# Performance work log

Measured on AMD Instinct MI355X. Metric: run time of the kernel, lower is better.

Reference implementation:

```python
import jax, jax.numpy as jnp
import numpy as np

B, S, D, H = 4, 4096, 128, 128

def setup_inputs() -> dict:
    key = jax.random.key(0)
    ks = jax.random.split(key, 7)
    sd = 1.0 / np.sqrt(D)
    return {
        "x": jax.random.normal(ks[0], (B, S, D), dtype=jnp.float32),
        "Wq": jax.random.normal(ks[1], (D, H), dtype=jnp.float32) * sd,
        "bq": jax.random.normal(ks[2], (H,), dtype=jnp.float32) * sd,
        "Wk": jax.random.normal(ks[3], (D, H), dtype=jnp.float32) * sd,
        "bk": jax.random.normal(ks[4], (H,), dtype=jnp.float32) * sd,
        "Wv": jax.random.normal(ks[5], (D, D), dtype=jnp.float32) * sd,
        "bv": jax.random.normal(ks[6], (D,), dtype=jnp.float32) * sd,
    }

def reference(x, Wq, bq, Wk, bk, Wv, bv):
    # Q,K: [B,S,H]; V: [B,S,D]
    Q = jnp.einsum('bsd,dh->bsh', x, Wq) + bq
    K = jnp.einsum('bsd,dh->bsh', x, Wk) + bk
    V = jnp.einsum('bsd,de->bse', x, Wv) + bv
    scale = jnp.sqrt(jnp.asarray(H, dtype=x.dtype))
    scores = jnp.einsum('bqh,bkh->bqk', Q, K) / scale  # [B,S,S]
    attn = jax.nn.softmax(scores, axis=-1)             # dropout = identity (eval mode)
    context = jnp.einsum('bqk,bkd->bqd', attn, V)      # [B,S,D]
    return context.mean(axis=1)                        # [B,D]
```

## Files before the change

### kernel.cpp

```cpp
#include <hip/hip_runtime.h>

#define SLEN 4096
#define DDIM 128
#define BATCH 4
#define KROWS 256
#define NKB (SLEN / KROWS)
#define QROWS 256
#define NQR (SLEN / QROWS)
#define NW 8
#define SCLOG2E 0.12751743f

typedef __bf16 v8bf __attribute__((ext_vector_type(8)));
typedef float f32x4 __attribute__((ext_vector_type(4)));

__device__ __forceinline__ f32x4 mfma16(v8bf a, v8bf b, f32x4 c) {
  return __builtin_amdgcn_mfma_f32_16x16x32_bf16(a, b, c, 0, 0, 0);
}

__device__ __forceinline__ void gload_lds16(const void* g, void* l) {
  __builtin_amdgcn_global_load_lds(
      (const __attribute__((address_space(1))) unsigned int*)g,
      (__attribute__((address_space(3))) unsigned int*)l, 16, 0, 0);
}

__device__ __forceinline__ void decode_bid(int bid, int& b, int& qr, int& kblk) {
  int x = bid & 7;
  int i = bid >> 3;
  int pr = x * 8 + (i >> 4);
  kblk = i & 15;
  b = pr >> 4;
  qr = pr & 15;
}

__device__ __forceinline__ void stage_kslab(const __bf16* __restrict__ Krow0,
                                            char* buf, int wave, int lane) {
#pragma unroll
  for (int it = 0; it < 8; ++it) {
    int s = it * 512 + wave * 64 + lane;
    int r = s >> 4;
    int pp = s & 15;
    int lsl = pp ^ (r & 7);
    const __bf16* src = Krow0 + (size_t)r * DDIM + lsl * 8;
    char* dst = buf + (size_t)(it * 512 + wave * 64) * 16;
    gload_lds16(src, dst);
  }
}

__device__ __forceinline__ void read4(v8bf k[4], const char* const pa[4], int t) {
  int off = t << 12;
#pragma unroll
  for (int h = 0; h < 4; ++h)
    k[h] = *reinterpret_cast<const v8bf*>(pa[h] + off);
}

__device__ __forceinline__ void mfma8(f32x4 A[2], const v8bf qf[2][4],
                                      const v8bf k[4]) {
  A[0] = (f32x4){0.f, 0.f, 0.f, 0.f};
  A[1] = (f32x4){0.f, 0.f, 0.f, 0.f};
#pragma unroll
  for (int h = 0; h < 4; ++h) {
    A[0] = mfma16(qf[0][h], k[h], A[0]);
    A[1] = mfma16(qf[1][h], k[h], A[1]);
  }
}

__device__ __forceinline__ void consume_z(const f32x4 A[2], float zacc[2][4]) {
#pragma unroll
  for (int qs = 0; qs < 2; ++qs)
#pragma unroll
    for (int j = 0; j < 4; ++j)
      zacc[qs][j] += exp2f(A[qs][j]);
}

__global__ __launch_bounds__(256) void k1_proj(const float* __restrict__ x,
                                               const float* __restrict__ Wq,
                                               const float* __restrict__ Wk,
                                               const float* __restrict__ bq,
                                               const float* __restrict__ bk,
                                               __bf16* __restrict__ Qb,
                                               __bf16* __restrict__ Kb) {
  int wave = threadIdx.x >> 6, lane = threadIdx.x & 63;
  int lr = lane & 15, lg = lane >> 4;

  __shared__ __align__(16) char wlds[64 * 1024];

#pragma unroll
  for (int it = 0; it < 16; ++it) {
    int idx = it * 256 + threadIdx.x;
    int ct = idx >> 8;
    int hs = (idx >> 6) & 3;
    int l  = idx & 63;
    int col = ((ct & 7) << 4) + (l & 15);
    const float* W = (ct < 8) ? Wq : Wk;
    int hbase = hs * 32 + (l >> 4) * 8;
    v8bf t;
#pragma unroll
    for (int i = 0; i < 8; ++i)
      t[i] = (__bf16)W[(hbase + i) * DDIM + col];
    *reinterpret_cast<v8bf*>(wlds + (size_t)idx * 16) = t;
  }

  int r0 = blockIdx.x * 64 + wave * 16;
  const float* xrow = x + (size_t)(r0 + lr) * DDIM;

  v8bf xf[4];
#pragma unroll
  for (int hs = 0; hs < 4; ++hs) {
    float4 a = *reinterpret_cast<const float4*>(xrow + hs * 32 + lg * 8);
    float4 c = *reinterpret_cast<const float4*>(xrow + hs * 32 + lg * 8 + 4);
    v8bf t;
    t[0] = (__bf16)a.x; t[1] = (__bf16)a.y; t[2] = (__bf16)a.z; t[3] = (__bf16)a.w;
    t[4] = (__bf16)c.x; t[5] = (__bf16)c.y; t[6] = (__bf16)c.z; t[7] = (__bf16)c.w;
    xf[hs] = t;
  }

  __syncthreads();

  for (int ct = 0; ct < 16; ++ct) {
    f32x4 acc = {0.f, 0.f, 0.f, 0.f};
#pragma unroll
    for (int hs = 0; hs < 4; ++hs) {
      v8bf wf = *reinterpret_cast<const v8bf*>(
          wlds + (size_t)((ct * 4 + hs) * 64 + lane) * 16);
      acc = mfma16(xf[hs], wf, acc);
    }
    int col = ((ct & 7) << 4) + lr;
    float bias = (ct < 8) ? bq[col] : bk[col];
    float sc   = (ct < 8) ? SCLOG2E : 1.0f;
    __bf16* dst = (ct < 8) ? Qb : Kb;
#pragma unroll
    for (int j = 0; j < 4; ++j) {
      int row = r0 + lg * 4 + j;
      dst[(size_t)row * DDIM + col] = (__bf16)((acc[j] + bias) * sc);
    }
  }
}

__global__ __launch_bounds__(512, 4) void k2a_z(const __bf16* __restrict__ Qb,
                                                const __bf16* __restrict__ Kb,
                                                float* __restrict__ zpart) {
  int b, qr, kblk;
  decode_bid(blockIdx.x, b, qr, kblk);
  int p = b * NQR + qr;
  int wave = threadIdx.x >> 6, lane = threadIdx.x & 63;
  int lr = lane & 15, lg = lane >> 4;

  __shared__ __align__(16) char kbuf[KROWS * 256];

  stage_kslab(Kb + ((size_t)b * SLEN + kblk * KROWS) * DDIM, kbuf, wave, lane);

  int qloc0 = wave * 32;
  const __bf16* Qp = Qb + ((size_t)b * SLEN + qr * QROWS + qloc0) * DDIM;

  v8bf qf[2][4];
#pragma unroll
  for (int qs = 0; qs < 2; ++qs)
#pragma unroll
    for (int hs = 0; hs < 4; ++hs)
      qf[qs][hs] = *reinterpret_cast<const v8bf*>(Qp + (size_t)(qs * 16 + lr) * DDIM + hs * 32 + lg * 8);

  const char* pa[4];
#pragma unroll
  for (int hs = 0; hs < 4; ++hs)
    pa[hs] = kbuf + lr * 256 + (((hs * 4 + lg) ^ (lr & 7)) << 4);

  float zacc[2][4];
#pragma unroll
  for (int qs = 0; qs < 2; ++qs)
#pragma unroll
    for (int j = 0; j < 4; ++j) zacc[qs][j] = 0.f;

  __syncthreads();

  v8bf kA[4], kB[4];
  f32x4 aA[2], aB[2];
  read4(kA, pa, 0);
  read4(kB, pa, 1);
  mfma8(aA, qf, kA);
#pragma unroll 1
  for (int i = 0; i < 7; ++i) {
    read4(kA, pa, 2 * i + 2);
    mfma8(aB, qf, kB);
    consume_z(aA, zacc);
    read4(kB, pa, 2 * i + 3);
    mfma8(aA, qf, kA);
    consume_z(aB, zacc);
  }
  mfma8(aB, qf, kB);
  consume_z(aA, zacc);
  consume_z(aB, zacc);

#pragma unroll
  for (int qs = 0; qs < 2; ++qs)
#pragma unroll
    for (int j = 0; j < 4; ++j) {
      float z = zacc[qs][j];
      z += __shfl_xor(z, 1);
      z += __shfl_xor(z, 2);
      z += __shfl_xor(z, 4);
      z += __shfl_xor(z, 8);
      if (lr == 0)
        zpart[((size_t)p * NKB + kblk) * QROWS + qloc0 + qs * 16 + lg * 4 + j] = z;
    }
}

__global__ __launch_bounds__(512, 4) void k2c_w(const __bf16* __restrict__ Qb,
                                                const __bf16* __restrict__ Kb,
                                                const float* __restrict__ zpart,
                                                float* __restrict__ wpart) {
  int b, qr, kblk;
  decode_bid(blockIdx.x, b, qr, kblk);
  int p = b * NQR + qr;
  int wave = threadIdx.x >> 6, lane = threadIdx.x & 63;
  int lr = lane & 15, lg = lane >> 4;

  __shared__ __align__(16) char kbuf[KROWS * 256];
  __shared__ float invZ[QROWS];
  __shared__ float warr[NW][KROWS];

  stage_kslab(Kb + ((size_t)b * SLEN + kblk * KROWS) * DDIM, kbuf, wave, lane);

  if (threadIdx.x < QROWS) {
    const float* zp = zpart + (size_t)p * NKB * QROWS + threadIdx.x;
    float z = 0.f;
#pragma unroll
    for (int kb = 0; kb < NKB; ++kb) z += zp[(size_t)kb * QROWS];
    invZ[threadIdx.x] = 1.0f / z;
  }
  __syncthreads();

  int qloc0 = wave * 32;
  const __bf16* Qp = Qb + ((size_t)b * SLEN + qr * QROWS + qloc0) * DDIM;

  v8bf qf[2][4];
#pragma unroll
  for (int qs = 0; qs < 2; ++qs)
#pragma unroll
    for (int hs = 0; hs < 4; ++hs)
      qf[qs][hs] = *reinterpret_cast<const v8bf*>(Qp + (size_t)(qs * 16 + lr) * DDIM + hs * 32 + lg * 8);

  float iz[2][4];
#pragma unroll
  for (int qs = 0; qs < 2; ++qs)
#pragma unroll
    for (int j = 0; j < 4; ++j)
      iz[qs][j] = invZ[qloc0 + qs * 16 + lg * 4 + j];

  const char* pa[4];
#pragma unroll
  for (int hs = 0; hs < 4; ++hs)
    pa[hs] = kbuf + lr * 256 + (((hs * 4 + lg) ^ (lr & 7)) << 4);

  float* wbase = &warr[wave][lr];

  auto cw = [&](const f32x4 A[2], int t) {
    float wk = 0.f;
#pragma unroll
    for (int qs = 0; qs < 2; ++qs)
#pragma unroll
      for (int j = 0; j < 4; ++j)
        wk += exp2f(A[qs][j]) * iz[qs][j];
    wk += __shfl_xor(wk, 16);
    wk += __shfl_xor(wk, 32);
    if (lg == 0) wbase[t * 16] = wk;
  };

  v8bf kA[4], kB[4];
  f32x4 aA[2], aB[2];
  read4(kA, pa, 0);
  read4(kB, pa, 1);
  mfma8(aA, qf, kA);
#pragma unroll 1
  for (int i = 0; i < 7; ++i) {
    read4(kA, pa, 2 * i + 2);
    mfma8(aB, qf, kB);
    cw(aA, 2 * i);
    read4(kB, pa, 2 * i + 3);
    mfma8(aA, qf, kA);
    cw(aB, 2 * i + 1);
  }
  mfma8(aB, qf, kB);
  cw(aA, 14);
  cw(aB, 15);

  __syncthreads();
  if (threadIdx.x < KROWS) {
    int k = threadIdx.x;
    float s = 0.f;
#pragma unroll
    for (int w = 0; w < NW; ++w) s += warr[w][k];
    wpart[(size_t)p * SLEN + kblk * KROWS + k] = s;
  }
}

__global__ __launch_bounds__(256) void k4_u(const float* __restrict__ x,
                                            const float* __restrict__ wpart,
                                            float* __restrict__ upart) {
  int b = blockIdx.y, kc = blockIdx.x;
  int t = threadIdx.x;
  __shared__ float ws[256];
  {
    const float* pw = wpart + (size_t)b * NQR * SLEN + kc * 256 + t;
    float s = 0.f;
#pragma unroll
    for (int j = 0; j < NQR; ++j) s += pw[(size_t)j * SLEN];
    ws[t] = s;
  }
  __syncthreads();
  int d = t & 127, kh = t >> 7;
  const float* xb = x + ((size_t)b * SLEN + kc * 256 + kh * 128) * DDIM;
  float acc = 0.f;
  for (int kk = 0; kk < 128; ++kk)
    acc += ws[kh * 128 + kk] * xb[(size_t)kk * DDIM + d];
  upart[((size_t)b * 32 + kc * 2 + kh) * DDIM + d] = acc;
}

__global__ __launch_bounds__(128) void k5_out(const float* __restrict__ upart,
                                              const float* __restrict__ Wv,
                                              const float* __restrict__ bv,
                                              float* __restrict__ out) {
  int b = blockIdx.x, d = threadIdx.x;
  __shared__ float u[DDIM];
  float s = 0.f;
  for (int c = 0; c < 32; ++c) s += upart[((size_t)b * 32 + c) * DDIM + d];
  u[d] = s;
  __syncthreads();
  float acc = 0.f;
  for (int dp = 0; dp < DDIM; ++dp) acc += u[dp] * Wv[(size_t)dp * DDIM + d];
  out[b * DDIM + d] = acc * (1.0f / SLEN) + bv[d];
}

extern "C" void kernel_launch(void* const* d_in, const int* in_sizes, int n_in,
                              void* d_out, int out_size, void* d_ws, size_t ws_size,
                              hipStream_t stream) {
  const float* x  = (const float*)d_in[0];
  const float* Wq = (const float*)d_in[1];
  const float* bq = (const float*)d_in[2];
  const float* Wk = (const float*)d_in[3];
  const float* bk = (const float*)d_in[4];
  const float* Wv = (const float*)d_in[5];
  const float* bv = (const float*)d_in[6];
  float* out = (float*)d_out;

  char* ws = (char*)d_ws;
  __bf16* Qb    = (__bf16*)(ws);
  __bf16* Kb    = (__bf16*)(ws + (4u << 20));
  float*  zpart = (float*)(ws + (8u << 20));
  float*  wpart = (float*)(ws + (9u << 20));
  float*  upart = (float*)(ws + (10u << 20));

  k1_proj<<<256, 256, 0, stream>>>(x, Wq, Wk, bq, bk, Qb, Kb);
  k2a_z  <<<NKB * NQR * BATCH, 512, 0, stream>>>(Qb, Kb, zpart);
  k2c_w  <<<NKB * NQR * BATCH, 512, 0, stream>>>(Qb, Kb, zpart, wpart);
  k4_u   <<<dim3(16, BATCH), 256, 0, stream>>>(x, wpart, upart);
  k5_out <<<BATCH, 128, 0, stream>>>(upart, Wv, bv, out);
}
```

Baseline: 72.63 us.

## Accumulate softmax denominators atomically and fuse final projection via last-block reduction

```diff
diff --git a/kernel.cpp b/kernel.cpp
--- a/kernel.cpp
+++ b/kernel.cpp
@@ -78,9 +78,14 @@
                                                const float* __restrict__ bq,
                                                const float* __restrict__ bk,
                                                __bf16* __restrict__ Qb,
-                                               __bf16* __restrict__ Kb) {
+                                               __bf16* __restrict__ Kb,
+                                               float* __restrict__ zsum,
+                                               unsigned int* __restrict__ done) {
   int wave = threadIdx.x >> 6, lane = threadIdx.x & 63;
   int lr = lane & 15, lg = lane >> 4;
+
+  if (threadIdx.x < 64) zsum[blockIdx.x * 64 + threadIdx.x] = 0.f;
+  if (blockIdx.x == 0 && threadIdx.x == 64) *done = 0u;
 
   __shared__ __align__(16) char wlds[64 * 1024];
 
@@ -138,7 +143,7 @@
 
 __global__ __launch_bounds__(512, 4) void k2a_z(const __bf16* __restrict__ Qb,
                                                 const __bf16* __restrict__ Kb,
-                                                float* __restrict__ zpart) {
+                                                float* __restrict__ zsum) {
   int b, qr, kblk;
   decode_bid(blockIdx.x, b, qr, kblk);
   int p = b * NQR + qr;
@@ -200,13 +205,13 @@
       z += __shfl_xor(z, 4);
       z += __shfl_xor(z, 8);
       if (lr == 0)
-        zpart[((size_t)p * NKB + kblk) * QROWS + qloc0 + qs * 16 + lg * 4 + j] = z;
+        atomicAdd(&zsum[(size_t)p * QROWS + qloc0 + qs * 16 + lg * 4 + j], z);
     }
 }
 
 __global__ __launch_bounds__(512, 4) void k2c_w(const __bf16* __restrict__ Qb,
                                                 const __bf16* __restrict__ Kb,
-                                                const float* __restrict__ zpart,
+                                                const float* __restrict__ zsum,
                                                 float* __restrict__ wpart) {
   int b, qr, kblk;
   decode_bid(blockIdx.x, b, qr, kblk);
@@ -220,13 +225,8 @@
 
   stage_kslab(Kb + ((size_t)b * SLEN + kblk * KROWS) * DDIM, kbuf, wave, lane);
 
-  if (threadIdx.x < QROWS) {
-    const float* zp = zpart + (size_t)p * NKB * QROWS + threadIdx.x;
-    float z = 0.f;
-#pragma unroll
-    for (int kb = 0; kb < NKB; ++kb) z += zp[(size_t)kb * QROWS];
-    invZ[threadIdx.x] = 1.0f / z;
-  }
+  if (threadIdx.x < QROWS)
+    invZ[threadIdx.x] = 1.0f / zsum[(size_t)p * QROWS + threadIdx.x];
   __syncthreads();
 
   int qloc0 = wave * 32;
@@ -293,9 +293,13 @@
   }
 }
 
-__global__ __launch_bounds__(256) void k4_u(const float* __restrict__ x,
-                                            const float* __restrict__ wpart,
-                                            float* __restrict__ upart) {
+__global__ __launch_bounds__(256) void k45_u(const float* __restrict__ x,
+                                             const float* __restrict__ wpart,
+                                             float* __restrict__ upart,
+                                             const float* __restrict__ Wv,
+                                             const float* __restrict__ bv,
+                                             float* __restrict__ out,
+                                             unsigned int* __restrict__ done) {
   int b = blockIdx.y, kc = blockIdx.x;
   int t = threadIdx.x;
   __shared__ float ws[256];
@@ -313,21 +317,34 @@
   for (int kk = 0; kk < 128; ++kk)
     acc += ws[kh * 128 + kk] * xb[(size_t)kk * DDIM + d];
   upart[((size_t)b * 32 + kc * 2 + kh) * DDIM + d] = acc;
-}
-
-__global__ __launch_bounds__(128) void k5_out(const float* __restrict__ upart,
-                                              const float* __restrict__ Wv,
-                                              const float* __restrict__ bv,
-                                              float* __restrict__ out) {
-  int b = blockIdx.x, d = threadIdx.x;
-  __shared__ float u[DDIM];
-  float s = 0.f;
-  for (int c = 0; c < 32; ++c) s += upart[((size_t)b * 32 + c) * DDIM + d];
-  u[d] = s;
-  __syncthreads();
-  float acc = 0.f;
-  for (int dp = 0; dp < DDIM; ++dp) acc += u[dp] * Wv[(size_t)dp * DDIM + d];
-  out[b * DDIM + d] = acc * (1.0f / SLEN) + bv[d];
+
+  __shared__ int isLast;
+  __syncthreads();
+  if (t == 0) {
+    __threadfence();
+    unsigned int v = atomicAdd(done, 1u);
+    isLast = (v == 63u);
+  }
+  __syncthreads();
+  if (!isLast) return;
+  __threadfence();
+
+  __shared__ float u[BATCH][DDIM];
+  for (int o = t; o < BATCH * DDIM; o += 256) {
+    int bb = o >> 7, dd = o & 127;
+    float s = 0.f;
+#pragma unroll
+    for (int c = 0; c < 32; ++c) s += upart[((size_t)bb * 32 + c) * DDIM + dd];
+    u[bb][dd] = s;
+  }
+  __syncthreads();
+  for (int o = t; o < BATCH * DDIM; o += 256) {
+    int bb = o >> 7, dd = o & 127;
+    float acc2 = 0.f;
+    for (int dp = 0; dp < DDIM; ++dp)
+      acc2 += u[bb][dp] * Wv[(size_t)dp * DDIM + dd];
+    out[bb * DDIM + dd] = acc2 * (1.0f / SLEN) + bv[dd];
+  }
 }
 
 extern "C" void kernel_launch(void* const* d_in, const int* in_sizes, int n_in,
@@ -345,13 +362,13 @@
   char* ws = (char*)d_ws;
   __bf16* Qb    = (__bf16*)(ws);
   __bf16* Kb    = (__bf16*)(ws + (4u << 20));
-  float*  zpart = (float*)(ws + (8u << 20));
+  float*  zsum  = (float*)(ws + (8u << 20));
+  unsigned int* done = (unsigned int*)(ws + (8u << 20) + (64u << 10));
   float*  wpart = (float*)(ws + (9u << 20));
   float*  upart = (float*)(ws + (10u << 20));
 
-  k1_proj<<<256, 256, 0, stream>>>(x, Wq, Wk, bq, bk, Qb, Kb);
-  k2a_z  <<<NKB * NQR * BATCH, 512, 0, stream>>>(Qb, Kb, zpart);
-  k2c_w  <<<NKB * NQR * BATCH, 512, 0, stream>>>(Qb, Kb, zpart, wpart);
-  k4_u   <<<dim3(16, BATCH), 256, 0, stream>>>(x, wpart, upart);
-  k5_out <<<BATCH, 128, 0, stream>>>(upart, Wv, bv, out);
-}
+  k1_proj<<<256, 256, 0, stream>>>(x, Wq, Wk, bq, bk, Qb, Kb, zsum, done);
+  k2a_z  <<<NKB * NQR * BATCH, 512, 0, stream>>>(Qb, Kb, zsum);
+  k2c_w  <<<NKB * NQR * BATCH, 512, 0, stream>>>(Qb, Kb, zsum, wpart);
+  k45_u  <<<dim3(16, BATCH), 256, 0, stream>>>(x, wpart, upart, Wv, bv, out, done);
+}
```

Result: slower. 80.80 us (+11.3%).
